# Kernel optimization log

Measured on AMD Instinct MI355X. Metric: run time of the kernel, lower is better.

## Reference

```python
import jax, jax.numpy as jnp
import numpy as np

N_NODES = 100000

def sage_conv(x, src, dst, Wl, bl, Wr):
    # PyG SAGEConv (mean aggr): out = lin_l(mean_{j in N(i)} x_j) + lin_r(x_i)
    msg = x[src]                                            # [E, d] gather
    agg = jax.ops.segment_sum(msg, dst, num_segments=N_NODES)
    cnt = jax.ops.segment_sum(jnp.ones((src.shape[0],), dtype=x.dtype), dst,
                              num_segments=N_NODES)
    agg = agg / jnp.maximum(cnt, 1.0)[:, None]              # mean over neighbors
    return agg @ Wl.T + bl + x @ Wr.T


def setup_inputs() -> dict:
    key = jax.random.key(0)
    ks = jax.random.split(key, 8)
    E = 1600000
    in_c, hid, out_c = 256, 128, 40
    x = jax.random.normal(ks[0], (N_NODES, in_c), dtype=jnp.float32)
    edge_index = jax.random.randint(ks[1], (2, E), 0, N_NODES, dtype=jnp.int64)
    s = 1.0 / np.sqrt(in_c)
    s2 = 1.0 / np.sqrt(hid)
    Wl1 = jax.random.uniform(ks[2], (hid, in_c), jnp.float32, -s, s)
    bl1 = jnp.zeros((hid,), jnp.float32)
    Wr1 = jax.random.uniform(ks[3], (hid, in_c), jnp.float32, -s, s)
    Wl2 = jax.random.uniform(ks[4], (out_c, hid), jnp.float32, -s2, s2)
    bl2 = jnp.zeros((out_c,), jnp.float32)
    Wr2 = jax.random.uniform(ks[5], (out_c, hid), jnp.float32, -s2, s2)
    return {"x": x, "edge_index": edge_index, "Wl1": Wl1, "bl1": bl1,
            "Wr1": Wr1, "Wl2": Wl2, "bl2": bl2, "Wr2": Wr2}


def reference(x, edge_index, Wl1, bl1, Wr1, Wl2, bl2, Wr2):
    src, dst = edge_index[0], edge_index[1]
    h = sage_conv(x, src, dst, Wl1, bl1, Wr1)
    h = jax.nn.relu(h)  # dropout is identity in eval mode
    h = sage_conv(h, src, dst, Wl2, bl2, Wr2)
    return jax.nn.log_softmax(h, axis=-1)
```

## Files before the change

### kernel.cpp

```cpp
#include <hip/hip_runtime.h>
#include <hip/hip_bf16.h>

#define N_NODES 100000
#define IN_C 256
#define HID 128
#define OUT_C 40

#define NPB 9
#define NPP (1 << NPB)
#define NPART ((N_NODES + NPP - 1) >> NPB)
#define CAP 16384

typedef short bf16x8 __attribute__((ext_vector_type(8)));
typedef float f32x4 __attribute__((ext_vector_type(4)));
typedef float f32x2 __attribute__((ext_vector_type(2)));

static __device__ __forceinline__ float bf2f(unsigned short u) {
    return __uint_as_float(((unsigned)u) << 16);
}
static __device__ __forceinline__ unsigned short f2bf(float f) {
    unsigned u = __float_as_uint(f);
    u += 0x7fffu + ((u >> 16) & 1u);
    return (unsigned short)(u >> 16);
}

__global__ __launch_bounds__(256) void cvtw_k(
    const float* __restrict__ Wl1, const float* __restrict__ Wr1,
    const float* __restrict__ Wl2, const float* __restrict__ Wr2,
    unsigned short* __restrict__ W1f, unsigned short* __restrict__ W2f)
{
    int gid = blockIdx.x * 256 + threadIdx.x;
    if (gid < 8192) {
        int g = gid;
        int ln = g & 63, blk = g >> 6;
        int c16 = blk >> 3, ks = blk & 7;
        int col = c16 * 16 + (ln & 15);
        int k0 = ks * 32 + (ln >> 4) * 8;
        const float* src = (col < 128) ? &Wl1[(size_t)col * 256 + k0]
                                       : &Wr1[(size_t)(col - 128) * 256 + k0];
        float4 v0 = *(const float4*)src;
        float4 v1 = *(const float4*)(src + 4);
        bf16x8 a;
        a[0] = (short)f2bf(v0.x); a[1] = (short)f2bf(v0.y);
        a[2] = (short)f2bf(v0.z); a[3] = (short)f2bf(v0.w);
        a[4] = (short)f2bf(v1.x); a[5] = (short)f2bf(v1.y);
        a[6] = (short)f2bf(v1.z); a[7] = (short)f2bf(v1.w);
        *(bf16x8*)&W1f[(size_t)g * 8] = a;
    } else if (gid < 9472) {
        int g = gid - 8192;
        int ln = g & 63, blk = g >> 6;
        int c16 = blk >> 2, ks = blk & 3;
        int col = c16 * 16 + (ln & 15);
        int k0 = ks * 32 + (ln >> 4) * 8;
        const float* src = (col < 40) ? &Wl2[(size_t)col * 128 + k0]
                                      : &Wr2[(size_t)(col - 40) * 128 + k0];
        float4 v0 = *(const float4*)src;
        float4 v1 = *(const float4*)(src + 4);
        bf16x8 a;
        a[0] = (short)f2bf(v0.x); a[1] = (short)f2bf(v0.y);
        a[2] = (short)f2bf(v0.z); a[3] = (short)f2bf(v0.w);
        a[4] = (short)f2bf(v1.x); a[5] = (short)f2bf(v1.y);
        a[6] = (short)f2bf(v1.z); a[7] = (short)f2bf(v1.w);
        *(bf16x8*)&W2f[(size_t)g * 8] = a;
    }
}

__global__ __launch_bounds__(256) void mega1_k(
    const int* __restrict__ ei, int E, int nblkS,
    int* __restrict__ pcnt, unsigned* __restrict__ pairs,
    const float* __restrict__ X,
    const unsigned short* __restrict__ Wf,
    const float* __restrict__ bias,
    unsigned* __restrict__ Yq,
    unsigned short* __restrict__ Zb,
    int M)
{
    constexpr int KP = 264;
    __shared__ unsigned short As[32][KP];
    const int bid = blockIdx.x;
    const int tx = threadIdx.x;

    if (bid < nblkS) {
        int* lh = (int*)&As[0][0];
        int* lb = lh + NPART;
        if (tx < NPART) lh[tx] = 0;
        __syncthreads();
        int base = bid * 4096;
        int n = min(4096, E - base);
        for (int i = tx; i < n; i += 256)
            atomicAdd(&lh[((unsigned)ei[E + base + i]) >> NPB], 1);
        __syncthreads();
        if (tx < NPART) {
            int c = lh[tx];
            lb[tx] = c ? atomicAdd(&pcnt[tx], c) : 0;
            lh[tx] = 0;
        }
        __syncthreads();
        for (int i = tx; i < n; i += 256) {
            unsigned src = (unsigned)ei[base + i];
            unsigned dst = (unsigned)ei[E + base + i];
            int p = dst >> NPB;
            int r = atomicAdd(&lh[p], 1);
            pairs[(size_t)p * CAP + lb[p] + r] = (src << NPB) | (dst & (NPP - 1));
        }
        return;
    }

    const int rowTile = (bid - nblkS) * 32;
    const int wc = tx >> 6, ln = tx & 63;
    const int lc = ln & 15, lk = (ln >> 4) * 8;

    float4 va[4], vb[4];
    #pragma unroll
    for (int i = 0; i < 4; ++i) {
        int g = i * 256 + tx;
        int r = g >> 5, kk = (g & 31) * 8;
        int gr = rowTile + r;
        if (gr < M) {
            const float* p = &X[(size_t)gr * 256 + kk];
            va[i] = *(const float4*)p;
            vb[i] = *(const float4*)(p + 4);
        } else {
            va[i] = make_float4(0.f, 0.f, 0.f, 0.f);
            vb[i] = make_float4(0.f, 0.f, 0.f, 0.f);
        }
    }
    #pragma unroll
    for (int i = 0; i < 4; ++i) {
        int g = i * 256 + tx;
        int r = g >> 5, kk = (g & 31) * 8;
        bf16x8 a;
        a[0] = (short)f2bf(va[i].x); a[1] = (short)f2bf(va[i].y);
        a[2] = (short)f2bf(va[i].z); a[3] = (short)f2bf(va[i].w);
        a[4] = (short)f2bf(vb[i].x); a[5] = (short)f2bf(vb[i].y);
        a[6] = (short)f2bf(vb[i].z); a[7] = (short)f2bf(vb[i].w);
        *(bf16x8*)&As[r][kk] = a;
    }
    __syncthreads();

    f32x4 acc[2][4] = {};
    #pragma unroll
    for (int ks = 0; ks < 8; ++ks) {
        int koff = ks * 32 + lk;
        bf16x8 bfr[4], af[2];
        #pragma unroll
        for (int n = 0; n < 4; ++n)
            bfr[n] = *(const bf16x8*)&Wf[(size_t)(((wc * 4 + n) * 8 + ks) * 512 + ln * 8)];
        #pragma unroll
        for (int m = 0; m < 2; ++m)
            af[m] = *(const bf16x8*)&As[m * 16 + lc][koff];
        #pragma unroll
        for (int m = 0; m < 2; ++m)
            #pragma unroll
            for (int n = 0; n < 4; ++n)
                acc[m][n] = __builtin_amdgcn_mfma_f32_16x16x32_bf16(af[m], bfr[n], acc[m][n], 0, 0, 0);
    }

    __syncthreads();
    const int lr4 = (ln >> 4) * 4;
    #pragma unroll
    for (int m = 0; m < 2; ++m) {
        int r0 = m * 16 + lr4;
        #pragma unroll
        for (int n = 0; n < 4; ++n) {
            int col = wc * 64 + n * 16 + lc;
            float b = (col >= 128) ? bias[col - 128] : 0.f;
            #pragma unroll
            for (int j = 0; j < 4; ++j)
                As[r0 + j][col] = f2bf(acc[m][n][j] + b);
        }
    }
    __syncthreads();
    #pragma unroll
    for (int i = 0; i < 4; ++i) {
        int g = i * 256 + tx;
        int r = g >> 5, c8 = (g & 31) * 8;
        int gr = rowTile + r;
        if (gr >= M) continue;
        bf16x8 v = *(const bf16x8*)&As[r][c8];
        if (c8 < 128) {
            float f0 = bf2f((unsigned short)v[0]), f1 = bf2f((unsigned short)v[1]);
            float f2 = bf2f((unsigned short)v[2]), f3 = bf2f((unsigned short)v[3]);
            float f4 = bf2f((unsigned short)v[4]), f5 = bf2f((unsigned short)v[5]);
            float f6 = bf2f((unsigned short)v[6]), f7 = bf2f((unsigned short)v[7]);
            unsigned lo = __builtin_amdgcn_cvt_pk_fp8_f32(f0, f1, 0, false);
            lo = __builtin_amdgcn_cvt_pk_fp8_f32(f2, f3, lo, true);
            unsigned hi = __builtin_amdgcn_cvt_pk_fp8_f32(f4, f5, 0, false);
            hi = __builtin_amdgcn_cvt_pk_fp8_f32(f6, f7, hi, true);
            uint2 o; o.x = lo; o.y = hi;
            *(uint2*)&Yq[(size_t)gr * 32 + (c8 >> 2)] = o;
        } else {
            *(bf16x8*)&Zb[(size_t)gr * 128 + (c8 - 128)] = v;
        }
    }
}

__global__ __launch_bounds__(256) void pbuild_k(const unsigned* __restrict__ pairs, const int* __restrict__ pcnt,
                                                unsigned* __restrict__ row_info, float* __restrict__ inv,
                                                int* __restrict__ csr, int N) {
    __shared__ int cnt[NPP];
    __shared__ int cur[NPP];
    __shared__ int wsum[4];
    int p = blockIdx.x;
    int ec = pcnt[p];
    size_t base = (size_t)p * CAP;
    int node0 = p << NPB;
    int tid = threadIdx.x;
    cnt[2 * tid] = 0; cnt[2 * tid + 1] = 0;
    __syncthreads();
    for (int e = tid; e < ec; e += 256)
        atomicAdd(&cnt[pairs[base + e] & (NPP - 1)], 1);
    __syncthreads();
    int c0 = cnt[2 * tid], c1 = cnt[2 * tid + 1];
    int s = c0 + c1;
    int lane = tid & 63, w = tid >> 6;
    int ps = s;
    #pragma unroll
    for (int off = 1; off < 64; off <<= 1) { int x = __shfl_up(ps, off); if (lane >= off) ps += x; }
    if (lane == 63) wsum[w] = ps;
    __syncthreads();
    int woff = 0;
    for (int i = 0; i < w; ++i) woff += wsum[i];
    int excl = woff + ps - s;
    int node = node0 + 2 * tid;
    int abeg = (int)base + excl;
    if (node < N) {
        row_info[node] = ((unsigned)abeg << 10) | (unsigned)min(c0, 1023);
        inv[node] = 1.f / fmaxf((float)c0, 1.f);
    }
    if (node + 1 < N) {
        row_info[node + 1] = ((unsigned)(abeg + c0) << 10) | (unsigned)min(c1, 1023);
        inv[node + 1] = 1.f / fmaxf((float)c1, 1.f);
    }
    cur[2 * tid] = excl; cur[2 * tid + 1] = excl + c0;
    __syncthreads();
    for (int e = tid; e < ec; e += 256) {
        unsigned pr = pairs[base + e];
        int r = atomicAdd(&cur[pr & (NPP - 1)], 1);
        csr[base + r] = (int)(pr >> NPB);
    }
}

__global__ __launch_bounds__(256) void gather1_k(const unsigned* __restrict__ row_info, const int* __restrict__ csr,
                                                 const unsigned* __restrict__ Yq,
                                                 unsigned short* __restrict__ Zb,
                                                 const float* __restrict__ inv, int n) {
    int node = blockIdx.x * 8 + (threadIdx.x >> 5);
    if (node >= n) return;
    int t = threadIdx.x & 31;
    unsigned info = row_info[node];
    int beg = (int)(info >> 10), end = beg + (int)(info & 1023);
    float a0 = 0.f, a1 = 0.f, a2 = 0.f, a3 = 0.f;
    int e = beg;
    for (; e + 4 <= end; e += 4) {
        int s0 = csr[e], s1 = csr[e + 1], s2 = csr[e + 2], s3 = csr[e + 3];
        unsigned u0 = Yq[(size_t)s0 * 32 + t];
        unsigned u1 = Yq[(size_t)s1 * 32 + t];
        unsigned u2 = Yq[(size_t)s2 * 32 + t];
        unsigned u3 = Yq[(size_t)s3 * 32 + t];
        f32x2 p;
        p = __builtin_amdgcn_cvt_pk_f32_fp8(u0, false); a0 += p[0]; a1 += p[1];
        p = __builtin_amdgcn_cvt_pk_f32_fp8(u0, true);  a2 += p[0]; a3 += p[1];
        p = __builtin_amdgcn_cvt_pk_f32_fp8(u1, false); a0 += p[0]; a1 += p[1];
        p = __builtin_amdgcn_cvt_pk_f32_fp8(u1, true);  a2 += p[0]; a3 += p[1];
        p = __builtin_amdgcn_cvt_pk_f32_fp8(u2, false); a0 += p[0]; a1 += p[1];
        p = __builtin_amdgcn_cvt_pk_f32_fp8(u2, true);  a2 += p[0]; a3 += p[1];
        p = __builtin_amdgcn_cvt_pk_f32_fp8(u3, false); a0 += p[0]; a1 += p[1];
        p = __builtin_amdgcn_cvt_pk_f32_fp8(u3, true);  a2 += p[0]; a3 += p[1];
    }
    for (; e < end; ++e) {
        unsigned u0 = Yq[(size_t)csr[e] * 32 + t];
        f32x2 p;
        p = __builtin_amdgcn_cvt_pk_f32_fp8(u0, false); a0 += p[0]; a1 += p[1];
        p = __builtin_amdgcn_cvt_pk_f32_fp8(u0, true);  a2 += p[0]; a3 += p[1];
    }
    float iv = inv[node];
    ushort4 z = *(const ushort4*)&Zb[(size_t)node * HID + t * 4];
    ushort4 h;
    h.x = f2bf(fmaxf(a0 * iv + bf2f(z.x), 0.f));
    h.y = f2bf(fmaxf(a1 * iv + bf2f(z.y), 0.f));
    h.z = f2bf(fmaxf(a2 * iv + bf2f(z.z), 0.f));
    h.w = f2bf(fmaxf(a3 * iv + bf2f(z.w), 0.f));
    *(ushort4*)&Zb[(size_t)node * HID + t * 4] = h;
}

__global__ __launch_bounds__(256) void gemm2_k(
    const unsigned short* __restrict__ Hb,
    const unsigned short* __restrict__ Wf,
    const float* __restrict__ bias,
    unsigned* __restrict__ Y2q,
    unsigned short* __restrict__ Z2b,
    int M)
{
    constexpr int KP = 136;
    __shared__ unsigned short As[128][KP];
    const int tx = threadIdx.x;
    const int rowTile = blockIdx.x * 128;
    const int wv = tx >> 6, ln = tx & 63;
    const int lc = ln & 15, lk = (ln >> 4) * 8;

    #pragma unroll
    for (int i = 0; i < 8; ++i) {
        int g = i * 256 + tx;
        int r = g >> 4, kk = (g & 15) * 8;
        int gr = rowTile + r;
        bf16x8 a = {};
        if (gr < M) a = *(const bf16x8*)&Hb[(size_t)gr * 128 + kk];
        *(bf16x8*)&As[r][kk] = a;
    }
    __syncthreads();

    f32x4 acc[2][5] = {};
    #pragma unroll
    for (int ks = 0; ks < 4; ++ks) {
        int koff = ks * 32 + lk;
        bf16x8 bfr[5], af[2];
        #pragma unroll
        for (int n = 0; n < 5; ++n)
            bfr[n] = *(const bf16x8*)&Wf[(size_t)((n * 4 + ks) * 512 + ln * 8)];
        #pragma unroll
        for (int m = 0; m < 2; ++m)
            af[m] = *(const bf16x8*)&As[wv * 32 + m * 16 + lc][koff];
        #pragma unroll
        for (int m = 0; m < 2; ++m)
            #pragma unroll
            for (int n = 0; n < 5; ++n)
                acc[m][n] = __builtin_amdgcn_mfma_f32_16x16x32_bf16(af[m], bfr[n], acc[m][n], 0, 0, 0);
    }

    __syncthreads();
    unsigned short (*OutL)[96] = (unsigned short (*)[96])&As[0][0];
    const int lr4 = (ln >> 4) * 4;
    #pragma unroll
    for (int m = 0; m < 2; ++m) {
        int r0 = wv * 32 + m * 16 + lr4;
        #pragma unroll
        for (int n = 0; n < 5; ++n) {
            int col = n * 16 + lc;
            float b = (col >= 40) ? bias[col - 40] : 0.f;
            #pragma unroll
            for (int j = 0; j < 4; ++j)
                OutL[r0 + j][col] = f2bf(acc[m][n][j] + b);
        }
    }
    __syncthreads();
    #pragma unroll
    for (int i = 0; i < 5; ++i) {
        int g = i * 256 + tx;
        int r = g / 10, cg = g % 10;
        int c8 = cg * 8;
        int gr = rowTile + r;
        if (gr >= M) continue;
        bf16x8 v = *(const bf16x8*)&OutL[r][c8];
        if (c8 < 40) {
            float f0 = bf2f((unsigned short)v[0]), f1 = bf2f((unsigned short)v[1]);
            float f2 = bf2f((unsigned short)v[2]), f3 = bf2f((unsigned short)v[3]);
            float f4 = bf2f((unsigned short)v[4]), f5 = bf2f((unsigned short)v[5]);
            float f6 = bf2f((unsigned short)v[6]), f7 = bf2f((unsigned short)v[7]);
            unsigned lo = __builtin_amdgcn_cvt_pk_fp8_f32(f0, f1, 0, false);
            lo = __builtin_amdgcn_cvt_pk_fp8_f32(f2, f3, lo, true);
            unsigned hi = __builtin_amdgcn_cvt_pk_fp8_f32(f4, f5, 0, false);
            hi = __builtin_amdgcn_cvt_pk_fp8_f32(f6, f7, hi, true);
            uint2 o; o.x = lo; o.y = hi;
            *(uint2*)&Y2q[(size_t)gr * 10 + (c8 >> 2)] = o;
        } else {
            *(bf16x8*)&Z2b[(size_t)gr * 40 + (c8 - 40)] = v;
        }
    }
}

__global__ __launch_bounds__(256) void gather2_logsm_k(const unsigned* __restrict__ row_info, const int* __restrict__ csr,
                                                       const unsigned* __restrict__ Y2q,
                                                       const unsigned short* __restrict__ Zb,
                                                       const float* __restrict__ inv,
                                                       float* __restrict__ out, int n) {
    int node = blockIdx.x * 16 + (threadIdx.x >> 4);
    if (node >= n) return;
    int t = threadIdx.x & 15;
    float4 v = make_float4(-INFINITY, -INFINITY, -INFINITY, -INFINITY);
    if (t < 10) {
        unsigned info = row_info[node];
        int beg = (int)(info >> 10), end = beg + (int)(info & 1023);
        float a0 = 0.f, a1 = 0.f, a2 = 0.f, a3 = 0.f;
        for (int e = beg; e < end; ++e) {
            unsigned u = Y2q[(size_t)csr[e] * 10 + t];
            f32x2 p;
            p = __builtin_amdgcn_cvt_pk_f32_fp8(u, false); a0 += p[0]; a1 += p[1];
            p = __builtin_amdgcn_cvt_pk_f32_fp8(u, true);  a2 += p[0]; a3 += p[1];
        }
        float iv = inv[node];
        ushort4 z = *(const ushort4*)&Zb[(size_t)node * OUT_C + t * 4];
        v.x = a0 * iv + bf2f(z.x); v.y = a1 * iv + bf2f(z.y);
        v.z = a2 * iv + bf2f(z.z); v.w = a3 * iv + bf2f(z.w);
    }
    float m = fmaxf(fmaxf(v.x, v.y), fmaxf(v.z, v.w));
    #pragma unroll
    for (int off = 8; off; off >>= 1) m = fmaxf(m, __shfl_xor(m, off, 16));
    float s4 = 0.f;
    if (t < 10) s4 = expf(v.x - m) + expf(v.y - m) + expf(v.z - m) + expf(v.w - m);
    #pragma unroll
    for (int off = 8; off; off >>= 1) s4 += __shfl_xor(s4, off, 16);
    float ls = m + logf(s4);
    if (t < 10) {
        float4 o;
        o.x = v.x - ls; o.y = v.y - ls; o.z = v.z - ls; o.w = v.w - ls;
        *(float4*)&out[(size_t)node * OUT_C + t * 4] = o;
    }
}

extern "C" void kernel_launch(void* const* d_in, const int* in_sizes, int n_in,
                              void* d_out, int out_size, void* d_ws, size_t ws_size,
                              hipStream_t stream) {
    const float* x   = (const float*)d_in[0];
    const int*   ei  = (const int*)d_in[1];
    const float* Wl1 = (const float*)d_in[2];
    const float* bl1 = (const float*)d_in[3];
    const float* Wr1 = (const float*)d_in[4];
    const float* Wl2 = (const float*)d_in[5];
    const float* bl2 = (const float*)d_in[6];
    const float* Wr2 = (const float*)d_in[7];
    float* out = (float*)d_out;
    const int N = N_NODES;
    const int E = in_sizes[1] / 2;

    char* ws = (char*)d_ws;
    int*      pcnt     = (int*)(ws + 0x0000);
    unsigned* row_info = (unsigned*)(ws + 0x10000);
    float*    inv      = (float*)(ws + 0x80000);
    int*      csr      = (int*)(ws + 0x100000);
    unsigned* pairs    = (unsigned*)(ws + 0xE00000);
    unsigned short* Z2b = (unsigned short*)(ws + 0xE00000);
    unsigned short* W1f = (unsigned short*)(ws + 0x1B00000);
    unsigned short* W2f = (unsigned short*)(ws + 0x1B60000);
    unsigned* Yq1   = (unsigned*)(ws + 0x1C00000);
    unsigned short* Z1b = (unsigned short*)(ws + 0x3500000);
    unsigned* Y2q   = (unsigned*)(ws + 0x5200000);

    hipMemsetAsync(pcnt, 0, NPART * 4, stream);

    cvtw_k<<<37, 256, 0, stream>>>(Wl1, Wr1, Wl2, Wr2, W1f, W2f);

    int nblkS = (E + 4095) / 4096;
    int nblkG = (N + 31) / 32;
    mega1_k<<<nblkS + nblkG, 256, 0, stream>>>(ei, E, nblkS, pcnt, pairs,
                                               x, W1f, bl1, Yq1, Z1b, N);

    pbuild_k<<<NPART, 256, 0, stream>>>(pairs, pcnt, row_info, inv, csr, N);

    gather1_k<<<N / 8, 256, 0, stream>>>(row_info, csr, Yq1, Z1b, inv, N);

    gemm2_k<<<(N + 127) / 128, 256, 0, stream>>>(Z1b, W2f, bl2, Y2q, Z2b, N);

    gather2_logsm_k<<<(N + 15) / 16, 256, 0, stream>>>(row_info, csr, Y2q, Z2b, inv, out, N);
}
```

Baseline: 186.7 us.

## Fuse layer-1 neighbor gather into layer-2 GEMM kernel via shared-memory staging

Merges the layer-1 aggregation kernel into the layer-2 GEMM kernel. Each 128-row block gathers and mean-reduces the fp8 neighbor features, adds the root term, applies ReLU and writes the bf16 hidden rows straight into shared memory before the MFMA GEMM. This removes one launch and the global write and re-read of the hidden activations. In exchange, the grid shrinks from about 12500 to about 782 blocks and each block does 16 serial gather iterations, which lowers the memory-level parallelism available to the latency-bound gather.

```diff
diff --git a/kernel.cpp b/kernel.cpp
--- a/kernel.cpp
+++ b/kernel.cpp
@@ -241,51 +241,11 @@
     }
 }
 
-__global__ __launch_bounds__(256) void gather1_k(const unsigned* __restrict__ row_info, const int* __restrict__ csr,
-                                                 const unsigned* __restrict__ Yq,
-                                                 unsigned short* __restrict__ Zb,
-                                                 const float* __restrict__ inv, int n) {
-    int node = blockIdx.x * 8 + (threadIdx.x >> 5);
-    if (node >= n) return;
-    int t = threadIdx.x & 31;
-    unsigned info = row_info[node];
-    int beg = (int)(info >> 10), end = beg + (int)(info & 1023);
-    float a0 = 0.f, a1 = 0.f, a2 = 0.f, a3 = 0.f;
-    int e = beg;
-    for (; e + 4 <= end; e += 4) {
-        int s0 = csr[e], s1 = csr[e + 1], s2 = csr[e + 2], s3 = csr[e + 3];
-        unsigned u0 = Yq[(size_t)s0 * 32 + t];
-        unsigned u1 = Yq[(size_t)s1 * 32 + t];
-        unsigned u2 = Yq[(size_t)s2 * 32 + t];
-        unsigned u3 = Yq[(size_t)s3 * 32 + t];
-        f32x2 p;
-        p = __builtin_amdgcn_cvt_pk_f32_fp8(u0, false); a0 += p[0]; a1 += p[1];
-        p = __builtin_amdgcn_cvt_pk_f32_fp8(u0, true);  a2 += p[0]; a3 += p[1];
-        p = __builtin_amdgcn_cvt_pk_f32_fp8(u1, false); a0 += p[0]; a1 += p[1];
-        p = __builtin_amdgcn_cvt_pk_f32_fp8(u1, true);  a2 += p[0]; a3 += p[1];
-        p = __builtin_amdgcn_cvt_pk_f32_fp8(u2, false); a0 += p[0]; a1 += p[1];
-        p = __builtin_amdgcn_cvt_pk_f32_fp8(u2, true);  a2 += p[0]; a3 += p[1];
-        p = __builtin_amdgcn_cvt_pk_f32_fp8(u3, false); a0 += p[0]; a1 += p[1];
-        p = __builtin_amdgcn_cvt_pk_f32_fp8(u3, true);  a2 += p[0]; a3 += p[1];
-    }
-    for (; e < end; ++e) {
-        unsigned u0 = Yq[(size_t)csr[e] * 32 + t];
-        f32x2 p;
-        p = __builtin_amdgcn_cvt_pk_f32_fp8(u0, false); a0 += p[0]; a1 += p[1];
-        p = __builtin_amdgcn_cvt_pk_f32_fp8(u0, true);  a2 += p[0]; a3 += p[1];
-    }
-    float iv = inv[node];
-    ushort4 z = *(const ushort4*)&Zb[(size_t)node * HID + t * 4];
-    ushort4 h;
-    h.x = f2bf(fmaxf(a0 * iv + bf2f(z.x), 0.f));
-    h.y = f2bf(fmaxf(a1 * iv + bf2f(z.y), 0.f));
-    h.z = f2bf(fmaxf(a2 * iv + bf2f(z.z), 0.f));
-    h.w = f2bf(fmaxf(a3 * iv + bf2f(z.w), 0.f));
-    *(ushort4*)&Zb[(size_t)node * HID + t * 4] = h;
-}
-
-__global__ __launch_bounds__(256) void gemm2_k(
-    const unsigned short* __restrict__ Hb,
+__global__ __launch_bounds__(256) void mega2_k(
+    const unsigned* __restrict__ row_info, const int* __restrict__ csr,
+    const unsigned* __restrict__ Yq,
+    const unsigned short* __restrict__ Zb,
+    const float* __restrict__ inv,
     const unsigned short* __restrict__ Wf,
     const float* __restrict__ bias,
     unsigned* __restrict__ Y2q,
@@ -296,20 +256,59 @@
     __shared__ unsigned short As[128][KP];
     const int tx = threadIdx.x;
     const int rowTile = blockIdx.x * 128;
+
+    {
+        const int grp = tx >> 5;
+        const int t = tx & 31;
+        #pragma unroll 1
+        for (int i = 0; i < 16; ++i) {
+            int r = i * 8 + grp;
+            int node = rowTile + r;
+            if (node >= M) {
+                ushort4 zz = make_ushort4(0, 0, 0, 0);
+                *(ushort4*)&As[r][t * 4] = zz;
+                continue;
+            }
+            unsigned info = row_info[node];
+            int beg = (int)(info >> 10), end = beg + (int)(info & 1023);
+            float a0 = 0.f, a1 = 0.f, a2 = 0.f, a3 = 0.f;
+            int e = beg;
+            for (; e + 4 <= end; e += 4) {
+                int s0 = csr[e], s1 = csr[e + 1], s2 = csr[e + 2], s3 = csr[e + 3];
+                unsigned u0 = Yq[(size_t)s0 * 32 + t];
+                unsigned u1 = Yq[(size_t)s1 * 32 + t];
+                unsigned u2 = Yq[(size_t)s2 * 32 + t];
+                unsigned u3 = Yq[(size_t)s3 * 32 + t];
+                f32x2 p;
+                p = __builtin_amdgcn_cvt_pk_f32_fp8(u0, false); a0 += p[0]; a1 += p[1];
+                p = __builtin_amdgcn_cvt_pk_f32_fp8(u0, true);  a2 += p[0]; a3 += p[1];
+                p = __builtin_amdgcn_cvt_pk_f32_fp8(u1, false); a0 += p[0]; a1 += p[1];
+                p = __builtin_amdgcn_cvt_pk_f32_fp8(u1, true);  a2 += p[0]; a3 += p[1];
+                p = __builtin_amdgcn_cvt_pk_f32_fp8(u2, false); a0 += p[0]; a1 += p[1];
+                p = __builtin_amdgcn_cvt_pk_f32_fp8(u2, true);  a2 += p[0]; a3 += p[1];
+                p = __builtin_amdgcn_cvt_pk_f32_fp8(u3, false); a0 += p[0]; a1 += p[1];
+                p = __builtin_amdgcn_cvt_pk_f32_fp8(u3, true);  a2 += p[0]; a3 += p[1];
+            }
+            for (; e < end; ++e) {
+                unsigned u0 = Yq[(size_t)csr[e] * 32 + t];
+                f32x2 p;
+                p = __builtin_amdgcn_cvt_pk_f32_fp8(u0, false); a0 += p[0]; a1 += p[1];
+                p = __builtin_amdgcn_cvt_pk_f32_fp8(u0, true);  a2 += p[0]; a3 += p[1];
+            }
+            float iv = inv[node];
+            ushort4 z = *(const ushort4*)&Zb[(size_t)node * HID + t * 4];
+            ushort4 h;
+            h.x = f2bf(fmaxf(a0 * iv + bf2f(z.x), 0.f));
+            h.y = f2bf(fmaxf(a1 * iv + bf2f(z.y), 0.f));
+            h.z = f2bf(fmaxf(a2 * iv + bf2f(z.z), 0.f));
+            h.w = f2bf(fmaxf(a3 * iv + bf2f(z.w), 0.f));
+            *(ushort4*)&As[r][t * 4] = h;
+        }
+    }
+    __syncthreads();
+
     const int wv = tx >> 6, ln = tx & 63;
     const int lc = ln & 15, lk = (ln >> 4) * 8;
-
-    #pragma unroll
-    for (int i = 0; i < 8; ++i) {
-        int g = i * 256 + tx;
-        int r = g >> 4, kk = (g & 15) * 8;
-        int gr = rowTile + r;
-        bf16x8 a = {};
-        if (gr < M) a = *(const bf16x8*)&Hb[(size_t)gr * 128 + kk];
-        *(bf16x8*)&As[r][kk] = a;
-    }
-    __syncthreads();
-
     f32x4 acc[2][5] = {};
     #pragma unroll
     for (int ks = 0; ks < 4; ++ks) {
@@ -447,9 +446,8 @@
 
     pbuild_k<<<NPART, 256, 0, stream>>>(pairs, pcnt, row_info, inv, csr, N);
 
-    gather1_k<<<N / 8, 256, 0, stream>>>(row_info, csr, Yq1, Z1b, inv, N);
-
-    gemm2_k<<<(N + 127) / 128, 256, 0, stream>>>(Z1b, W2f, bl2, Y2q, Z2b, N);
+    mega2_k<<<(N + 127) / 128, 256, 0, stream>>>(row_info, csr, Yq1, Z1b, inv,
+                                                 W2f, bl2, Y2q, Z2b, N);
 
     gather2_logsm_k<<<(N + 15) / 16, 256, 0, stream>>>(row_info, csr, Y2q, Z2b, inv, out, N);
 }
```

Measured after the change: 219.5 us. 1.18x slower.
